# Kernel tuning notes

Measured on AMD Instinct MI355X. Metric: run time of the kernel, lower is better.

The kernel has to match this reference:

```python
import jax, jax.numpy as jnp
import numpy as np

D_MODEL, N_HEADS = 768, 12
D_K = D_MODEL // N_HEADS
NEG = -1e9


def setup_inputs() -> dict:
    key = jax.random.key(0)
    ks = jax.random.split(key, 12)
    B, S, D = 2, 4096, D_MODEL
    s = 1.0 / np.sqrt(D)
    inp = {
        'query': jax.random.normal(ks[0], (B, S, D), jnp.float32),
        'key': jax.random.normal(ks[1], (B, S, D), jnp.float32),
        'value': jax.random.normal(ks[2], (B, S, D), jnp.float32),
        'mask': jnp.ones((B, S), jnp.int32),
        'Wq': jax.random.normal(ks[3], (D, D), jnp.float32) * s,
        'bq': jnp.zeros((D,), jnp.float32),
        'Wk': jax.random.normal(ks[4], (D, D), jnp.float32) * s,
        'bk': jnp.zeros((D,), jnp.float32),
        'Wv': jax.random.normal(ks[5], (D, D), jnp.float32) * s,
        'bv': jnp.zeros((D,), jnp.float32),
        'Wo': jax.random.normal(ks[6], (D, D), jnp.float32) * s,
        'bo': jnp.zeros((D,), jnp.float32),
    }
    return inp


def reference(query, key, value, mask, Wq, bq, Wk, bk, Wv, bv, Wo, bo):
    B, Sq, D = query.shape
    Sk = key.shape[1]
    # torch Linear: x @ W.T + b; weights stored [out, in]
    def proj(x, W, b, S):
        return (x @ W.T + b).reshape(B, S, N_HEADS, D_K).transpose(0, 2, 1, 3)
    Q = proj(query, Wq, bq, Sq)   # [B,H,Sq,Dk]
    K = proj(key, Wk, bk, Sk)
    V = proj(value, Wv, bv, Sk)
    scores = jnp.einsum('bhqd,bhkd->bhqk', Q, K) / jnp.sqrt(jnp.float32(D_K))
    # padding mask on keys: [B,1,1,Sk]
    scores = jnp.where(mask[:, None, None, :] == 0, NEG, scores)
    # causal mask (triu, diagonal=1)
    causal = jnp.triu(jnp.ones((Sq, Sk), bool), k=1)
    scores = jnp.where(causal[None, None], NEG, scores)
    attn = jax.nn.softmax(scores, axis=-1)
    out = jnp.einsum('bhqk,bhkd->bhqd', attn, V)
    out = out.transpose(0, 2, 1, 3).reshape(B, Sq, D)
    return out @ Wo.T + bo
```

## Files before the change

kernel.cpp:

```cpp
#include <hip/hip_runtime.h>
#include <hip/hip_bf16.h>

#define D_MODEL 768
#define N_HEADS 12
#define D_K     64
#define NEG_INF (-1e9f)
#define SCALE_Q 0.1803368801111154f
#define W_ELEMS (D_MODEL * D_MODEL)
#define PS_PAD  40
#define RED_PAD 36

typedef __attribute__((ext_vector_type(8))) short          bf16x8;
typedef __attribute__((ext_vector_type(4))) float          floatx4;
typedef __attribute__((ext_vector_type(4))) unsigned short ushortx4;
typedef __attribute__((ext_vector_type(2))) unsigned int   uintx2;

static __device__ __forceinline__ unsigned short f2bf(float f) {
    unsigned u = __builtin_bit_cast(unsigned, f);
    u += 0x7FFFu + ((u >> 16) & 1u);
    return (unsigned short)(u >> 16);
}

static __device__ __forceinline__ void gload_lds16(const void* g, void* l) {
    __builtin_amdgcn_global_load_lds(
        (const __attribute__((address_space(1))) void*)g,
        (__attribute__((address_space(3))) void*)l, 16, 0, 0);
}

__global__ __launch_bounds__(256) void convert_w4(
    const float* __restrict__ W0, const float* __restrict__ W1,
    const float* __restrict__ W2, const float* __restrict__ W3,
    unsigned short* __restrict__ out)
{
    const float* src[4] = {W0, W1, W2, W3};
    const float* W = src[blockIdx.y];
    unsigned short* o = out + (size_t)blockIdx.y * W_ELEMS;
    const int i = (blockIdx.x * 256 + threadIdx.x) * 4;
    float4 v = *(const float4*)(W + i);
    ushortx4 h = { f2bf(v.x), f2bf(v.y), f2bf(v.z), f2bf(v.w) };
    *(ushortx4*)(o + i) = h;
}

__global__ __launch_bounds__(256) void convert_a3(
    const float* __restrict__ A0, const float* __restrict__ A1,
    const float* __restrict__ A2,
    unsigned short* __restrict__ O0, unsigned short* __restrict__ O1,
    unsigned short* __restrict__ O2)
{
    const int z = blockIdx.y;
    const float* A = (z == 0) ? A0 : (z == 1) ? A1 : A2;
    unsigned short* O = (z == 0) ? O0 : (z == 1) ? O1 : O2;
    const int i = (blockIdx.x * 256 + threadIdx.x) * 4;
    float4 v = *(const float4*)(A + i);
    ushortx4 h = { f2bf(v.x), f2bf(v.y), f2bf(v.z), f2bf(v.w) };
    *(ushortx4*)(O + i) = h;
}

template <int TM, bool QKV>
__global__ __launch_bounds__(256) void gemm_bt(
    const unsigned short* __restrict__ A0, const unsigned short* __restrict__ A1,
    const unsigned short* __restrict__ A2,
    const unsigned short* __restrict__ W0, const unsigned short* __restrict__ W1,
    const unsigned short* __restrict__ W2,
    const float* __restrict__ b0, const float* __restrict__ b1,
    const float* __restrict__ b2,
    void* __restrict__ C0, void* __restrict__ C1, void* __restrict__ C2,
    int S)
{
    constexpr int NI = TM / 32;
    __shared__ __align__(16) unsigned short As[TM * 32];
    __shared__ __align__(16) unsigned short Bs[128 * 32];

    const int z = QKV ? blockIdx.z : 0;
    const unsigned short* A = (z == 0) ? A0 : (z == 1) ? A1 : A2;
    const unsigned short* W = (z == 0) ? W0 : (z == 1) ? W1 : W2;
    const float* bias       = (z == 0) ? b0 : (z == 1) ? b1 : b2;
    void* C                 = (z == 0) ? C0 : (z == 1) ? C1 : C2;
    const float scale = (QKV && z == 0) ? SCALE_Q : 1.0f;
    const int mode = QKV ? ((z == 2) ? 3 : 1) : 0;

    const int tid  = threadIdx.x;
    const int wave = tid >> 6;
    const int lane = tid & 63;
    const int quad = lane >> 4;
    const int l16  = lane & 15;
    const int m0 = blockIdx.x * TM;
    const int n0 = blockIdx.y * 128;
    const int wm = (wave & 1) * (TM / 2);
    const int wn = (wave >> 1) * 64;
    const int sr = lane >> 2;
    const int sc = (lane & 3) << 3;

    const floatx4 zero4 = {0.f, 0.f, 0.f, 0.f};
    floatx4 acc[NI][4];
    #pragma unroll
    for (int i = 0; i < NI; ++i)
        #pragma unroll
        for (int j = 0; j < 4; ++j) acc[i][j] = zero4;

    for (int k0 = 0; k0 < D_MODEL; k0 += 32) {
        #pragma unroll
        for (int c = 0; c < TM / 64; ++c) {
            const int row = wave * (TM / 4) + c * 16;
            gload_lds16(A + (size_t)(m0 + row + sr) * D_MODEL + k0 + sc,
                        As + row * 32);
        }
        #pragma unroll
        for (int c = 0; c < 2; ++c) {
            const int row = wave * 32 + c * 16;
            gload_lds16(W + (size_t)(n0 + row + sr) * D_MODEL + k0 + sc,
                        Bs + row * 32);
        }
        __syncthreads();

        bf16x8 af[NI], bfr[4];
        #pragma unroll
        for (int i = 0; i < NI; ++i)
            af[i] = *(const bf16x8*)(As + (wm + i * 16 + l16) * 32 + quad * 8);
        #pragma unroll
        for (int j = 0; j < 4; ++j)
            bfr[j] = *(const bf16x8*)(Bs + (wn + j * 16 + l16) * 32 + quad * 8);
        #pragma unroll
        for (int i = 0; i < NI; ++i)
            #pragma unroll
            for (int j = 0; j < 4; ++j)
                acc[i][j] = __builtin_amdgcn_mfma_f32_16x16x32_bf16(
                    bfr[j], af[i], acc[i][j], 0, 0, 0);
        __syncthreads();
    }

    #pragma unroll
    for (int i = 0; i < NI; ++i) {
        const int m = m0 + wm + i * 16 + l16;
        #pragma unroll
        for (int j = 0; j < 4; ++j) {
            const int nb = n0 + wn + j * 16 + quad * 4;
            const float4 bv = *(const float4*)(bias + nb);
            float v0 = (acc[i][j][0] + bv.x) * scale;
            float v1 = (acc[i][j][1] + bv.y) * scale;
            float v2 = (acc[i][j][2] + bv.z) * scale;
            float v3 = (acc[i][j][3] + bv.w) * scale;
            if (mode == 0) {
                float4 o = {v0, v1, v2, v3};
                *(float4*)((float*)C + (size_t)m * D_MODEL + nb) = o;
            } else if (mode == 1) {
                ushortx4 o = {f2bf(v0), f2bf(v1), f2bf(v2), f2bf(v3)};
                *(ushortx4*)((unsigned short*)C + (size_t)m * D_MODEL + nb) = o;
            } else {
                const int bb = m / S, s = m - bb * S;
                const int hh = nb >> 6, d = nb & 63;
                unsigned short* base = (unsigned short*)C +
                    ((size_t)(bb * N_HEADS + hh) * D_K + d) * S + s;
                base[0]             = f2bf(v0);
                base[(size_t)S]     = f2bf(v1);
                base[(size_t)S * 2] = f2bf(v2);
                base[(size_t)S * 3] = f2bf(v3);
            }
        }
    }
}

union FlashSmem {
    struct {
        unsigned short KsF[8 * 512];
        unsigned short VtsF[8 * 512];
        unsigned short Ps[4][32 * PS_PAD];
    } kv;
    struct {
        float red[2][64 * RED_PAD];
        float redl[2][32];
    } ep;
};

__global__ __launch_bounds__(256, 5) void flash_attn(
    const unsigned short* __restrict__ Qp,
    const unsigned short* __restrict__ Kp,
    const unsigned short* __restrict__ VpT,
    const int* __restrict__ mask,
    unsigned short* __restrict__ O,
    int S)
{
    __shared__ __align__(16) FlashSmem sm;
    __shared__ __align__(16) float mskf[64];

    const int L  = blockIdx.x;
    const int bh = L % 24;
    const int nqt = S >> 6;
    const int qt = (nqt - 1) - (L / 24);
    const int h  = bh % 12;
    const int b  = bh / 12;
    const int tid  = threadIdx.x;
    const int wave = tid >> 6;
    const int qw   = wave & 1;
    const int kw   = wave >> 1;
    const int lane = tid & 63;
    const int quad = lane >> 4;
    const int l16  = lane & 15;

    const int q0 = qt * 64;
    const int qs = q0 + qw * 32;

    const unsigned short* Kbase = Kp  + (size_t)(b * S) * D_MODEL + h * D_K;
    const unsigned short* Vbase = VpT + (size_t)(b * N_HEADS + h) * D_K * S;

    const floatx4 zero4 = {0.f, 0.f, 0.f, 0.f};
    const short one_bf = (short)0x3F80;
    const bf16x8 ones = {one_bf, one_bf, one_bf, one_bf,
                         one_bf, one_bf, one_bf, one_bf};

    bf16x8 qf[2][2];
    #pragma unroll
    for (int qg = 0; qg < 2; ++qg) {
        const size_t rowQ = (size_t)(b * S + qs + qg * 16 + l16) * D_MODEL + h * D_K;
        qf[qg][0] = *(const bf16x8*)(Qp + rowQ + quad * 8);
        qf[qg][1] = *(const bf16x8*)(Qp + rowQ + 32 + quad * 8);
    }

    floatx4 accO[2][4];
    floatx4 accL[2];
    #pragma unroll
    for (int qg = 0; qg < 2; ++qg) {
        accL[qg] = zero4;
        #pragma unroll
        for (int dt = 0; dt < 4; ++dt) accO[qg][dt] = zero4;
    }

    unsigned short* Psw = sm.kv.Ps[wave];

    for (int kt = 0; kt <= qt; ++kt) {
        const int k0 = kt * 64;
        #pragma unroll
        for (int c = 0; c < 2; ++c) {
            gload_lds16(Kbase + (size_t)(k0 + wave * 16 + l16) * D_MODEL + c * 32 + quad * 8,
                        sm.kv.KsF + (wave * 2 + c) * 512);
            gload_lds16(Vbase + (size_t)(wave * 16 + l16) * S + k0 + c * 32 + quad * 8,
                        sm.kv.VtsF + (wave * 2 + c) * 512);
        }
        if (tid < 64)
            mskf[tid] = (mask[b * S + k0 + tid] == 0) ? NEG_INF : 0.f;
        __syncthreads();

        const bool skip = (kt == qt) && (kw == 1) && (qw == 0);
        if (!skip) {
            const bool diag = (kt == qt) && (kw == qw);
            const int kb = k0 + kw * 32;

            #pragma unroll
            for (int nt = 0; nt < 2; ++nt) {
                const floatx4 minit = *(const floatx4*)(mskf + kw * 32 + nt * 16 + quad * 4);
                const int kgf = (kw * 2 + nt) * 2;
                const bf16x8 kf0 = *(const bf16x8*)(sm.kv.KsF + kgf * 512 + lane * 8);
                const bf16x8 kf1 = *(const bf16x8*)(sm.kv.KsF + (kgf + 1) * 512 + lane * 8);
                #pragma unroll
                for (int qg = 0; qg < 2; ++qg) {
                    floatx4 c = minit;
                    c = __builtin_amdgcn_mfma_f32_16x16x32_bf16(kf0, qf[qg][0], c, 0, 0, 0);
                    c = __builtin_amdgcn_mfma_f32_16x16x32_bf16(kf1, qf[qg][1], c, 0, 0, 0);
                    if (diag) {
                        const int kk = kb + nt * 16 + quad * 4;
                        const int qq = qs + qg * 16 + l16;
                        #pragma unroll
                        for (int r = 0; r < 4; ++r)
                            if (kk + r > qq) c[r] = NEG_INF;
                    }
                    const float e0 = __builtin_exp2f(c[0]);
                    const float e1 = __builtin_exp2f(c[1]);
                    const float e2 = __builtin_exp2f(c[2]);
                    const float e3 = __builtin_exp2f(c[3]);
                    uintx2 pk;
                    pk[0] = __builtin_amdgcn_perm(__builtin_bit_cast(unsigned, e1),
                                                  __builtin_bit_cast(unsigned, e0), 0x07060302u);
                    pk[1] = __builtin_amdgcn_perm(__builtin_bit_cast(unsigned, e3),
                                                  __builtin_bit_cast(unsigned, e2), 0x07060302u);
                    *(uintx2*)(Psw + (qg * 16 + l16) * PS_PAD + nt * 16 + quad * 4) = pk;
                }
            }

            bf16x8 vf[4];
            #pragma unroll
            for (int dt = 0; dt < 4; ++dt)
                vf[dt] = *(const bf16x8*)(sm.kv.VtsF + (dt * 2 + kw) * 512 + lane * 8);
            #pragma unroll
            for (int qg = 0; qg < 2; ++qg) {
                const bf16x8 pf = *(const bf16x8*)(Psw + (qg * 16 + l16) * PS_PAD + quad * 8);
                #pragma unroll
                for (int dt = 0; dt < 4; ++dt)
                    accO[qg][dt] = __builtin_amdgcn_mfma_f32_16x16x32_bf16(
                        pf, vf[dt], accO[qg][dt], 0, 0, 0);
                accL[qg] = __builtin_amdgcn_mfma_f32_16x16x32_bf16(
                    pf, ones, accL[qg], 0, 0, 0);
            }
        }
        __syncthreads();
    }

    if (kw == 1) {
        float* rb = sm.ep.red[qw];
        #pragma unroll
        for (int qg = 0; qg < 2; ++qg) {
            #pragma unroll
            for (int dt = 0; dt < 4; ++dt)
                *(floatx4*)(rb + (dt * 16 + l16) * RED_PAD + qg * 16 + quad * 4) = accO[qg][dt];
            if (l16 == 0)
                *(floatx4*)(sm.ep.redl[qw] + qg * 16 + quad * 4) = accL[qg];
        }
    }
    __syncthreads();
    if (kw == 0) {
        const float* rb = sm.ep.red[qw];
        #pragma unroll
        for (int qg = 0; qg < 2; ++qg) {
            accL[qg] += *(const floatx4*)(sm.ep.redl[qw] + qg * 16 + quad * 4);
            #pragma unroll
            for (int dt = 0; dt < 4; ++dt)
                accO[qg][dt] += *(const floatx4*)(rb + (dt * 16 + l16) * RED_PAD + qg * 16 + quad * 4);
            #pragma unroll
            for (int r = 0; r < 4; ++r) {
                const float inv = 1.f / accL[qg][r];
                const int gq = qs + qg * 16 + quad * 4 + r;
                unsigned short* ob = O + (size_t)(b * S + gq) * D_MODEL + h * D_K;
                #pragma unroll
                for (int dt = 0; dt < 4; ++dt)
                    ob[dt * 16 + l16] = f2bf(accO[qg][dt][r] * inv);
            }
        }
    }
}

extern "C" void kernel_launch(void* const* d_in, const int* in_sizes, int n_in,
                              void* d_out, int out_size, void* d_ws, size_t ws_size,
                              hipStream_t stream) {
    const float* query = (const float*)d_in[0];
    const float* key   = (const float*)d_in[1];
    const float* value = (const float*)d_in[2];
    const int*   mask  = (const int*)d_in[3];
    const float* Wq = (const float*)d_in[4];
    const float* bq = (const float*)d_in[5];
    const float* Wk = (const float*)d_in[6];
    const float* bk = (const float*)d_in[7];
    const float* Wv = (const float*)d_in[8];
    const float* bv = (const float*)d_in[9];
    const float* Wo = (const float*)d_in[10];
    const float* bo = (const float*)d_in[11];

    const int B  = 2;
    const int BS = in_sizes[3];
    const int S  = BS / B;
    const int M  = BS;

    unsigned short* Qp  = (unsigned short*)d_ws;
    unsigned short* Kp  = Qp  + (size_t)M * D_MODEL;
    unsigned short* VpT = Kp  + (size_t)M * D_MODEL;
    unsigned short* Obf = VpT + (size_t)M * D_MODEL;
    unsigned short* Wbf = Obf + (size_t)M * D_MODEL;
    unsigned short* Wqb = Wbf;
    unsigned short* Wkb = Wbf + (size_t)W_ELEMS;
    unsigned short* Wvb = Wbf + (size_t)W_ELEMS * 2;
    unsigned short* Wob = Wbf + (size_t)W_ELEMS * 3;
    unsigned short* ka = (unsigned short*)d_out;
    unsigned short* va = ka + (size_t)M * D_MODEL;

    dim3 blk(256);
    convert_w4<<<dim3(W_ELEMS / 1024, 4), blk, 0, stream>>>(Wq, Wk, Wv, Wo, Wbf);
    convert_a3<<<dim3((M * D_MODEL) / 1024, 3), blk, 0, stream>>>(
        query, key, value, Obf, ka, va);

    gemm_bt<128, true><<<dim3(M / 128, D_MODEL / 128, 3), blk, 0, stream>>>(
        Obf, ka, va, Wqb, Wkb, Wvb, bq, bk, bv, Qp, Kp, VpT, S);

    flash_attn<<<24 * (S / 64), blk, 0, stream>>>(Qp, Kp, VpT, mask, Obf, S);

    gemm_bt<64, false><<<dim3(M / 64, D_MODEL / 128, 1), blk, 0, stream>>>(
        Obf, Obf, Obf, Wob, Wob, Wob, bo, bo, bo,
        d_out, d_out, d_out, S);
}
```

Measured before the change: 352.3 us.

## Load K/V fragments directly from global memory, drop LDS staging and block barriers

The flash attention loop no longer stages K and V tiles into LDS with a barrier. Each wave now loads its own K, V and mask fragments straight from global into registers and skips the fully masked diagonal tile early. This removes two __syncthreads per tile and the LDS round trip, but each wave re-reads data from global memory or cache without sharing it across waves. Register pressure goes up, so launch bounds drop from 5 to 4 blocks per CU.

New measurement: 402.8 us. +14.3%, slower.

```diff
diff --git a/kernel.cpp b/kernel.cpp
--- a/kernel.cpp
+++ b/kernel.cpp
@@ -161,18 +161,14 @@
 }
 
 union FlashSmem {
-    struct {
-        unsigned short KsF[8 * 512];
-        unsigned short VtsF[8 * 512];
-        unsigned short Ps[4][32 * PS_PAD];
-    } kv;
+    unsigned short Ps[4][32 * PS_PAD];
     struct {
         float red[2][64 * RED_PAD];
         float redl[2][32];
     } ep;
 };
 
-__global__ __launch_bounds__(256, 5) void flash_attn(
+__global__ __launch_bounds__(256, 4) void flash_attn(
     const unsigned short* __restrict__ Qp,
     const unsigned short* __restrict__ Kp,
     const unsigned short* __restrict__ VpT,
@@ -181,7 +177,6 @@
     int S)
 {
     __shared__ __align__(16) FlashSmem sm;
-    __shared__ __align__(16) float mskf[64];
 
     const int L  = blockIdx.x;
     const int bh = L % 24;
@@ -202,6 +197,7 @@
 
     const unsigned short* Kbase = Kp  + (size_t)(b * S) * D_MODEL + h * D_K;
     const unsigned short* Vbase = VpT + (size_t)(b * N_HEADS + h) * D_K * S;
+    const int* maskb = mask + b * S;
 
     const floatx4 zero4 = {0.f, 0.f, 0.f, 0.f};
     const short one_bf = (short)0x3F80;
@@ -225,75 +221,75 @@
         for (int dt = 0; dt < 4; ++dt) accO[qg][dt] = zero4;
     }
 
-    unsigned short* Psw = sm.kv.Ps[wave];
+    unsigned short* Psw = sm.Ps[wave];
 
     for (int kt = 0; kt <= qt; ++kt) {
+        if ((kt == qt) && (kw == 1) && (qw == 0)) continue;
         const int k0 = kt * 64;
-        #pragma unroll
-        for (int c = 0; c < 2; ++c) {
-            gload_lds16(Kbase + (size_t)(k0 + wave * 16 + l16) * D_MODEL + c * 32 + quad * 8,
-                        sm.kv.KsF + (wave * 2 + c) * 512);
-            gload_lds16(Vbase + (size_t)(wave * 16 + l16) * S + k0 + c * 32 + quad * 8,
-                        sm.kv.VtsF + (wave * 2 + c) * 512);
-        }
-        if (tid < 64)
-            mskf[tid] = (mask[b * S + k0 + tid] == 0) ? NEG_INF : 0.f;
-        __syncthreads();
-
-        const bool skip = (kt == qt) && (kw == 1) && (qw == 0);
-        if (!skip) {
-            const bool diag = (kt == qt) && (kw == qw);
-            const int kb = k0 + kw * 32;
-
-            #pragma unroll
-            for (int nt = 0; nt < 2; ++nt) {
-                const floatx4 minit = *(const floatx4*)(mskf + kw * 32 + nt * 16 + quad * 4);
-                const int kgf = (kw * 2 + nt) * 2;
-                const bf16x8 kf0 = *(const bf16x8*)(sm.kv.KsF + kgf * 512 + lane * 8);
-                const bf16x8 kf1 = *(const bf16x8*)(sm.kv.KsF + (kgf + 1) * 512 + lane * 8);
-                #pragma unroll
-                for (int qg = 0; qg < 2; ++qg) {
-                    floatx4 c = minit;
-                    c = __builtin_amdgcn_mfma_f32_16x16x32_bf16(kf0, qf[qg][0], c, 0, 0, 0);
-                    c = __builtin_amdgcn_mfma_f32_16x16x32_bf16(kf1, qf[qg][1], c, 0, 0, 0);
-                    if (diag) {
-                        const int kk = kb + nt * 16 + quad * 4;
-                        const int qq = qs + qg * 16 + l16;
-                        #pragma unroll
-                        for (int r = 0; r < 4; ++r)
-                            if (kk + r > qq) c[r] = NEG_INF;
-                    }
-                    const float e0 = __builtin_exp2f(c[0]);
-                    const float e1 = __builtin_exp2f(c[1]);
-                    const float e2 = __builtin_exp2f(c[2]);
-                    const float e3 = __builtin_exp2f(c[3]);
-                    uintx2 pk;
-                    pk[0] = __builtin_amdgcn_perm(__builtin_bit_cast(unsigned, e1),
-                                                  __builtin_bit_cast(unsigned, e0), 0x07060302u);
-                    pk[1] = __builtin_amdgcn_perm(__builtin_bit_cast(unsigned, e3),
-                                                  __builtin_bit_cast(unsigned, e2), 0x07060302u);
-                    *(uintx2*)(Psw + (qg * 16 + l16) * PS_PAD + nt * 16 + quad * 4) = pk;
+        const int kb = k0 + kw * 32;
+        const bool diag = (kt == qt) && (kw == qw);
+
+        bf16x8 kf[2][2];
+        #pragma unroll
+        for (int nt = 0; nt < 2; ++nt) {
+            const unsigned short* kr = Kbase + (size_t)(kb + nt * 16 + l16) * D_MODEL;
+            kf[nt][0] = *(const bf16x8*)(kr + quad * 8);
+            kf[nt][1] = *(const bf16x8*)(kr + 32 + quad * 8);
+        }
+        bf16x8 vf[4];
+        #pragma unroll
+        for (int dt = 0; dt < 4; ++dt)
+            vf[dt] = *(const bf16x8*)(Vbase + (size_t)(dt * 16 + l16) * S + kb + quad * 8);
+        int4 mi[2];
+        #pragma unroll
+        for (int nt = 0; nt < 2; ++nt)
+            mi[nt] = *(const int4*)(maskb + kb + nt * 16 + quad * 4);
+
+        #pragma unroll
+        for (int nt = 0; nt < 2; ++nt) {
+            floatx4 minit;
+            minit[0] = (mi[nt].x == 0) ? NEG_INF : 0.f;
+            minit[1] = (mi[nt].y == 0) ? NEG_INF : 0.f;
+            minit[2] = (mi[nt].z == 0) ? NEG_INF : 0.f;
+            minit[3] = (mi[nt].w == 0) ? NEG_INF : 0.f;
+            #pragma unroll
+            for (int qg = 0; qg < 2; ++qg) {
+                floatx4 c = minit;
+                c = __builtin_amdgcn_mfma_f32_16x16x32_bf16(kf[nt][0], qf[qg][0], c, 0, 0, 0);
+                c = __builtin_amdgcn_mfma_f32_16x16x32_bf16(kf[nt][1], qf[qg][1], c, 0, 0, 0);
+                if (diag) {
+                    const int kk = kb + nt * 16 + quad * 4;
+                    const int qq = qs + qg * 16 + l16;
+                    #pragma unroll
+                    for (int r = 0; r < 4; ++r)
+                        if (kk + r > qq) c[r] = NEG_INF;
                 }
+                const float e0 = __builtin_exp2f(c[0]);
+                const float e1 = __builtin_exp2f(c[1]);
+                const float e2 = __builtin_exp2f(c[2]);
+                const float e3 = __builtin_exp2f(c[3]);
+                uintx2 pk;
+                pk[0] = __builtin_amdgcn_perm(__builtin_bit_cast(unsigned, e1),
+                                              __builtin_bit_cast(unsigned, e0), 0x07060302u);
+                pk[1] = __builtin_amdgcn_perm(__builtin_bit_cast(unsigned, e3),
+                                              __builtin_bit_cast(unsigned, e2), 0x07060302u);
+                *(uintx2*)(Psw + (qg * 16 + l16) * PS_PAD + nt * 16 + quad * 4) = pk;
             }
-
-            bf16x8 vf[4];
+        }
+
+        #pragma unroll
+        for (int qg = 0; qg < 2; ++qg) {
+            const bf16x8 pf = *(const bf16x8*)(Psw + (qg * 16 + l16) * PS_PAD + quad * 8);
             #pragma unroll
             for (int dt = 0; dt < 4; ++dt)
-                vf[dt] = *(const bf16x8*)(sm.kv.VtsF + (dt * 2 + kw) * 512 + lane * 8);
-            #pragma unroll
-            for (int qg = 0; qg < 2; ++qg) {
-                const bf16x8 pf = *(const bf16x8*)(Psw + (qg * 16 + l16) * PS_PAD + quad * 8);
-                #pragma unroll
-                for (int dt = 0; dt < 4; ++dt)
-                    accO[qg][dt] = __builtin_amdgcn_mfma_f32_16x16x32_bf16(
-                        pf, vf[dt], accO[qg][dt], 0, 0, 0);
-                accL[qg] = __builtin_amdgcn_mfma_f32_16x16x32_bf16(
-                    pf, ones, accL[qg], 0, 0, 0);
-            }
-        }
-        __syncthreads();
-    }
-
+                accO[qg][dt] = __builtin_amdgcn_mfma_f32_16x16x32_bf16(
+                    pf, vf[dt], accO[qg][dt], 0, 0, 0);
+            accL[qg] = __builtin_amdgcn_mfma_f32_16x16x32_bf16(
+                pf, ones, accL[qg], 0, 0, 0);
+        }
+    }
+
+    __syncthreads();
     if (kw == 1) {
         float* rb = sm.ep.red[qw];
         #pragma unroll
```
